# Optimization experiments

Hardware: AMD Instinct MI355X
Metric: run time of the kernel (lower is better)

## Reference

```python
import jax, jax.numpy as jnp
import numpy as np

DIM = 1024
HEADS = 16
HEAD_DIM = DIM // HEADS
EPS = 1e-6


def setup_inputs() -> dict:
    key = jax.random.key(0)
    ks = jax.random.split(key, 4)
    x = jax.random.normal(ks[0], (2, 2048, DIM), dtype=jnp.float32)
    W_qkv = jax.random.normal(ks[1], (3 * DIM, DIM), dtype=jnp.float32) * (DIM ** -0.5)
    q_gamma = jnp.ones((HEAD_DIM,), jnp.float32)
    q_beta = jnp.zeros((HEAD_DIM,), jnp.float32)
    k_gamma = jnp.ones((HEAD_DIM,), jnp.float32)
    k_beta = jnp.zeros((HEAD_DIM,), jnp.float32)
    W_proj = jax.random.normal(ks[2], (DIM, DIM), dtype=jnp.float32) * (DIM ** -0.5)
    b_proj = jnp.zeros((DIM,), jnp.float32)
    return {"x": x, "W_qkv": W_qkv, "q_gamma": q_gamma, "q_beta": q_beta,
            "k_gamma": k_gamma, "k_beta": k_beta, "W_proj": W_proj, "b_proj": b_proj}


def _layernorm(x, gamma, beta):
    mu = jnp.mean(x, axis=-1, keepdims=True)
    var = jnp.mean(jnp.square(x - mu), axis=-1, keepdims=True)
    return (x - mu) * jax.lax.rsqrt(var + EPS) * gamma + beta


def reference(x, W_qkv, q_gamma, q_beta, k_gamma, k_beta, W_proj, b_proj):
    B, N, C = x.shape
    H, D = HEADS, HEAD_DIM
    scale = D ** -0.5
    qkv = jnp.einsum('bnc,oc->bno', x, W_qkv)            # [B,N,3C]
    qkv = qkv.reshape(B, N, 3, H, D).transpose(2, 0, 3, 1, 4)  # [3,B,H,N,D]
    q, k, v = qkv[0], qkv[1], qkv[2]
    q = _layernorm(q, q_gamma, q_beta)
    k = _layernorm(k, k_gamma, k_beta)
    attn = jnp.einsum('bhnd,bhmd->bhnm', q * scale, k)   # [B,H,N,N]
    attn = jax.nn.softmax(attn, axis=-1)
    out = jnp.einsum('bhnm,bhmd->bhnd', attn, v)         # [B,H,N,D]
    out = out.transpose(0, 2, 1, 3).reshape(B, N, C)
    return jnp.einsum('bnc,oc->bno', out, W_proj) + b_proj
```

## Files before the change

### kernel.cpp

```cpp
#include <hip/hip_runtime.h>

#define DIM 1024
#define HEADS 16
#define HD 64
#define BATCH 2
#define SEQ 2048
#define ROWS (BATCH*SEQ)
#define EPS 1e-6f

typedef float f32x4  __attribute__((ext_vector_type(4)));
typedef float f32x16 __attribute__((ext_vector_type(16)));
typedef short s16x4  __attribute__((ext_vector_type(4)));
typedef short s16x8  __attribute__((ext_vector_type(8)));

static __device__ __forceinline__ short f2bf(float f) {
    union { float f; unsigned u; } x; x.f = f;
    unsigned r = x.u + 0x7FFFu + ((x.u >> 16) & 1u);
    return (short)(r >> 16);
}
static __device__ __forceinline__ s16x8 pack8(float4 lo, float4 hi) {
    s16x8 r;
    r[0]=f2bf(lo.x); r[1]=f2bf(lo.y); r[2]=f2bf(lo.z); r[3]=f2bf(lo.w);
    r[4]=f2bf(hi.x); r[5]=f2bf(hi.y); r[6]=f2bf(hi.z); r[7]=f2bf(hi.w);
    return r;
}
static __device__ __forceinline__ unsigned cvtpk(float a, float b) {
    unsigned r;
    asm("v_cvt_pk_bf16_f32 %0, %1, %2" : "=v"(r) : "v"(a), "v"(b));
    return r;
}
static __device__ __forceinline__ void gld16(short* l, const short* g) {
    __builtin_amdgcn_global_load_lds(
        (const __attribute__((address_space(1))) void*)g,
        (__attribute__((address_space(3))) void*)l, 16, 0, 0);
}

#define MFMA32(A,B,C) __builtin_amdgcn_mfma_f32_32x32x16_bf16(A, B, C, 0, 0, 0)
#define MFMA16(A,B,C) __builtin_amdgcn_mfma_f32_16x16x32_bf16(A, B, C, 0, 0, 0)

__global__ __launch_bounds__(256) void convert3(
    const float* __restrict__ x, const float* __restrict__ wq,
    const float* __restrict__ wp,
    short* __restrict__ xb, short* __restrict__ wqb, short* __restrict__ wpb)
{
    const int idx = blockIdx.x * 256 + threadIdx.x;
    const int C1 = 4194304/8, C2 = 3145728/8;
    const float* src; short* dst; int off;
    if (idx < C1)            { src = x;  dst = xb;  off = idx; }
    else if (idx < C1 + C2)  { src = wq; dst = wqb; off = idx - C1; }
    else                     { src = wp; dst = wpb; off = idx - C1 - C2; }
    float4 a = ((const float4*)src)[off*2];
    float4 b = ((const float4*)src)[off*2 + 1];
    ((s16x8*)dst)[off] = pack8(a, b);
}

#define BKG 64

template<int MODE>
__global__ __launch_bounds__(256) void gemm_bf16(
    const short* __restrict__ A, const short* __restrict__ W,
    const float* __restrict__ bias,
    const float* __restrict__ qg, const float* __restrict__ qbeta,
    const float* __restrict__ kg, const float* __restrict__ kbeta,
    short* __restrict__ qb, short* __restrict__ kb, short* __restrict__ vb,
    float* __restrict__ out)
{
    alignas(16) __shared__ short As[128*BKG];
    alignas(16) __shared__ short Bs[128*BKG];
    const int tid  = threadIdx.x;
    const int lane = tid & 63, wave = tid >> 6;
    const int wr = wave >> 1, wc = wave & 1;
    const int c = lane & 15, g = lane >> 4;
    const int brow = blockIdx.y * 128, bcol = blockIdx.x * 128;

    const int srow = lane >> 3;
    const int scol = (lane & 7) * 8;
    const short* ag = A + (size_t)(brow + srow)*DIM + scol;
    const short* wg = W + (size_t)(bcol + srow)*DIM + scol;

    f32x4 acc[4][4] = {};

    for (int k0 = 0; k0 < DIM; k0 += BKG) {
        #pragma unroll
        for (int j = 0; j < 4; j++) {
            const int rg = (wave*4 + j) * 8;
            gld16(&As[rg*BKG], ag + (size_t)rg*DIM + k0);
            gld16(&Bs[rg*BKG], wg + (size_t)rg*DIM + k0);
        }
        __syncthreads();

        #pragma unroll
        for (int ks = 0; ks < 2; ks++) {
            s16x8 af[4], bf[4];
            #pragma unroll
            for (int m = 0; m < 4; m++)
                af[m] = *(const s16x8*)&As[(wr*64 + m*16 + c)*BKG + ks*32 + g*8];
            #pragma unroll
            for (int n = 0; n < 4; n++)
                bf[n] = *(const s16x8*)&Bs[(wc*64 + n*16 + c)*BKG + ks*32 + g*8];
            #pragma unroll
            for (int m = 0; m < 4; m++)
                #pragma unroll
                for (int n = 0; n < 4; n++)
                    acc[m][n] = MFMA16(af[m], bf[n], acc[m][n]);
        }
        __syncthreads();
    }

    if (MODE == 0) {
        const int colbase = bcol + wc*64;
        const int t = colbase >> 10;
        const int h = (colbase >> 6) & 15;
        short* dst = (t == 0) ? qb : (t == 1) ? kb : vb;
        float gam[4], bet[4];
        float scale = 1.0f;
        if (t < 2) {
            const float* G  = (t == 0) ? qg : kg;
            const float* Bt = (t == 0) ? qbeta : kbeta;
            #pragma unroll
            for (int n = 0; n < 4; n++) { gam[n] = G[n*16 + c]; bet[n] = Bt[n*16 + c]; }
            if (t == 0) scale = 0.125f * 1.44269504088896340736f;
        }
        #pragma unroll
        for (int m = 0; m < 4; m++) {
            #pragma unroll
            for (int j = 0; j < 4; j++) {
                const int row = brow + wr*64 + m*16 + g*4 + j;
                const int bi = row >> 11, ni = row & (SEQ-1);
                const size_t rb = ((size_t)(bi*HEADS + h)*SEQ + ni)*HD;
                float v0 = acc[m][0][j], v1 = acc[m][1][j];
                float v2 = acc[m][2][j], v3 = acc[m][3][j];
                if (t < 2) {
                    float s = (v0 + v1) + (v2 + v3);
                    s += __shfl_xor(s, 1); s += __shfl_xor(s, 2);
                    s += __shfl_xor(s, 4); s += __shfl_xor(s, 8);
                    const float mu = s * 0.015625f;
                    v0 -= mu; v1 -= mu; v2 -= mu; v3 -= mu;
                    float vv = (v0*v0 + v1*v1) + (v2*v2 + v3*v3);
                    vv += __shfl_xor(vv, 1); vv += __shfl_xor(vv, 2);
                    vv += __shfl_xor(vv, 4); vv += __shfl_xor(vv, 8);
                    const float rstd = rsqrtf(vv * 0.015625f + EPS);
                    v0 = (v0*rstd*gam[0] + bet[0]) * scale;
                    v1 = (v1*rstd*gam[1] + bet[1]) * scale;
                    v2 = (v2*rstd*gam[2] + bet[2]) * scale;
                    v3 = (v3*rstd*gam[3] + bet[3]) * scale;
                }
                dst[rb + 0*16 + c] = f2bf(v0);
                dst[rb + 1*16 + c] = f2bf(v1);
                dst[rb + 2*16 + c] = f2bf(v2);
                dst[rb + 3*16 + c] = f2bf(v3);
            }
        }
    } else {
        #pragma unroll
        for (int n = 0; n < 4; n++) {
            const int col = bcol + wc*64 + n*16 + c;
            const float bv = bias[col];
            #pragma unroll
            for (int m = 0; m < 4; m++) {
                #pragma unroll
                for (int j = 0; j < 4; j++) {
                    const int row = brow + wr*64 + m*16 + g*4 + j;
                    out[(size_t)row*DIM + col] = acc[m][n][j] + bv;
                }
            }
        }
    }
}

__global__ __launch_bounds__(256) void vtrans(
    const short* __restrict__ vin, short* __restrict__ vt)
{
    constexpr int LT = 72;
    alignas(16) __shared__ short T[64*LT];
    const int bh = blockIdx.x, n0 = blockIdx.y * 64;
    const int t = threadIdx.x;
    const int r = t >> 2, cq = (t & 3) * 16;
    const short* src = vin + ((size_t)bh*SEQ + n0 + r)*HD + cq;
    *(s16x8*)&T[r*LT + cq]     = *(const s16x8*)src;
    *(s16x8*)&T[r*LT + cq + 8] = *(const s16x8*)(src + 8);
    __syncthreads();
    const int d = t >> 2, nq = (t & 3) * 16;
    s16x8 a, b;
    #pragma unroll
    for (int e = 0; e < 8; e++) { a[e] = T[(nq+e)*LT + d]; b[e] = T[(nq+8+e)*LT + d]; }
    short* dst = vt + ((size_t)bh*HD + d)*SEQ + n0 + nq;
    *(s16x8*)dst       = a;
    *(s16x8*)(dst + 8) = b;
}

__global__ __launch_bounds__(512, 4) void attn_kernel(
    const short* __restrict__ qbuf, const short* __restrict__ kbuf,
    const short* __restrict__ vtbuf, short* __restrict__ aout)
{
    alignas(16) __shared__ short Ks[2][2][64*64];
    alignas(16) __shared__ short Vs[2][2][64*64];

    const int bh = blockIdx.x;
    const int tid = threadIdx.x;
    const int wave = tid >> 6, lane = tid & 63;
    const int half = wave >> 2, w4 = wave & 3;
    const int l31 = lane & 31, hi = lane >> 5;
    const int q0 = (blockIdx.y * 4 + w4) * 32;
    const size_t base = (size_t)bh * SEQ * HD;
    const short* Q  = qbuf  + base;
    const short* K  = kbuf  + base;
    const short* VT = vtbuf + base;
    const int kt0 = half * (SEQ/2);

    const int t2 = tid & 255;
    const int srow = t2 >> 2;
    const int scol = (t2 & 3) * 16;
    const int sd0 = (srow*128 + scol*2) ^ ((srow & 7) << 4);
    const int sd1 = sd0 ^ 16;

    s16x8 qf[4];
    const short* qrow = Q + (size_t)(q0 + l31)*HD + 8*hi;
    #pragma unroll
    for (int ks = 0; ks < 4; ks++) qf[ks] = *(const s16x8*)(qrow + 16*ks);

    int roff[8];
    #pragma unroll
    for (int ks = 0; ks < 4; ks++) {
        roff[ks]   = (l31*128      + 32*ks + 16*hi) ^ ((l31 & 7) << 4);
        roff[4+ks] = ((32+l31)*128 + 32*ks + 16*hi) ^ ((l31 & 7) << 4);
    }

    f32x16 o0 = {}, o1 = {};
    float m = -1e30f, l = 0.f;

    {
        const short* kg = K  + (size_t)(kt0 + srow)*HD + scol;
        const short* vg = VT + (size_t)srow*SEQ + kt0 + scol;
        s16x8 ka = *(const s16x8*)kg, kb2 = *(const s16x8*)(kg + 8);
        s16x8 va = *(const s16x8*)vg, vb2 = *(const s16x8*)(vg + 8);
        *(s16x8*)((char*)Ks[half][0] + sd0) = ka;
        *(s16x8*)((char*)Ks[half][0] + sd1) = kb2;
        *(s16x8*)((char*)Vs[half][0] + sd0) = va;
        *(s16x8*)((char*)Vs[half][0] + sd1) = vb2;
    }
    __syncthreads();

    int cur = 0;
    for (int i = 0; i < 16; i++) {
        const int ktn = kt0 + ((i + 1) & 15) * 64;
        const short* kg = K  + (size_t)(ktn + srow)*HD + scol;
        const short* vg = VT + (size_t)srow*SEQ + ktn + scol;
        s16x8 ka = *(const s16x8*)kg, kb2 = *(const s16x8*)(kg + 8);
        s16x8 va = *(const s16x8*)vg, vb2 = *(const s16x8*)(vg + 8);

        const char* kl = (const char*)Ks[half][cur];
        const char* vl = (const char*)Vs[half][cur];

        f32x16 s0 = {}, s1 = {};
        __builtin_amdgcn_s_setprio(1);
        #pragma unroll
        for (int ks = 0; ks < 4; ks++) {
            s16x8 kf0 = *(const s16x8*)(kl + roff[ks]);
            s16x8 kf1 = *(const s16x8*)(kl + roff[4+ks]);
            s0 = MFMA32(kf0, qf[ks], s0);
            s1 = MFMA32(kf1, qf[ks], s1);
        }
        __builtin_amdgcn_s_setprio(0);

        float t8[8];
        #pragma unroll
        for (int i2 = 0; i2 < 8; i2++) t8[i2] = fmaxf(fmaxf(s0[i2], s0[i2+8]), fmaxf(s1[i2], s1[i2+8]));
        #pragma unroll
        for (int i2 = 0; i2 < 4; i2++) t8[i2] = fmaxf(t8[i2], t8[i2+4]);
        float pmax = fmaxf(fmaxf(t8[0], t8[2]), fmaxf(t8[1], t8[3]));
        pmax = fmaxf(pmax, __shfl_xor(pmax, 32));

        if (!__all(pmax - m <= 8.0f)) {
            float mn = fmaxf(m, pmax);
            float corr = exp2f(m - mn);
            #pragma unroll
            for (int i2 = 0; i2 < 16; i2++) { o0[i2] *= corr; o1[i2] *= corr; }
            l *= corr;
            m = mn;
        }
        #pragma unroll
        for (int i2 = 0; i2 < 16; i2++) {
            s0[i2] = exp2f(s0[i2] - m);
            s1[i2] = exp2f(s1[i2] - m);
        }
        float a8[8];
        #pragma unroll
        for (int i2 = 0; i2 < 8; i2++) a8[i2] = (s0[i2] + s0[i2+8]) + (s1[i2] + s1[i2+8]);
        #pragma unroll
        for (int i2 = 0; i2 < 4; i2++) a8[i2] += a8[i2+4];
        float rs = (a8[0] + a8[2]) + (a8[1] + a8[3]);
        rs += __shfl_xor(rs, 32);
        l += rs;

        s16x8 pa[4];
        #pragma unroll
        for (int ks = 0; ks < 4; ks++) {
            const int rb = 8*(ks & 1);
            unsigned A0, A1, B0, B1;
            if (ks < 2) {
                A0 = cvtpk(s0[rb+0], s0[rb+1]); A1 = cvtpk(s0[rb+2], s0[rb+3]);
                B0 = cvtpk(s0[rb+4], s0[rb+5]); B1 = cvtpk(s0[rb+6], s0[rb+7]);
            } else {
                A0 = cvtpk(s1[rb+0], s1[rb+1]); A1 = cvtpk(s1[rb+2], s1[rb+3]);
                B0 = cvtpk(s1[rb+4], s1[rb+5]); B1 = cvtpk(s1[rb+6], s1[rb+7]);
            }
            asm volatile("v_permlane32_swap_b32 %0, %1" : "+v"(A0), "+v"(B0));
            asm volatile("v_permlane32_swap_b32 %0, %1" : "+v"(A1), "+v"(B1));
            union { s16x8 v; unsigned u[4]; } w;
            w.u[0] = A0; w.u[1] = A1; w.u[2] = B0; w.u[3] = B1;
            pa[ks] = w.v;
        }

        __builtin_amdgcn_s_setprio(1);
        #pragma unroll
        for (int ks = 0; ks < 4; ks++) {
            s16x8 vf0 = *(const s16x8*)(vl + roff[ks]);
            s16x8 vf1 = *(const s16x8*)(vl + roff[4+ks]);
            o0 = MFMA32(vf0, pa[ks], o0);
            o1 = MFMA32(vf1, pa[ks], o1);
        }
        __builtin_amdgcn_s_setprio(0);

        const int nxt = cur ^ 1;
        *(s16x8*)((char*)Ks[half][nxt] + sd0) = ka;
        *(s16x8*)((char*)Ks[half][nxt] + sd1) = kb2;
        *(s16x8*)((char*)Vs[half][nxt] + sd0) = va;
        *(s16x8*)((char*)Vs[half][nxt] + sd1) = vb2;
        __syncthreads();
        cur = nxt;
    }

    float* OL = (float*)&Ks[0][0][0];
    float* ML = (float*)&Vs[0][0][0];

    if (half == 1) {
        float* ob = OL + ((size_t)(w4*64 + lane))*32;
        #pragma unroll
        for (int i = 0; i < 8; i++) {
            const int slot = (i + (lane & 7)) & 7;
            f32x4 v;
            if (i < 4) { v[0]=o0[4*i]; v[1]=o0[4*i+1]; v[2]=o0[4*i+2]; v[3]=o0[4*i+3]; }
            else { const int j = i-4; v[0]=o1[4*j]; v[1]=o1[4*j+1]; v[2]=o1[4*j+2]; v[3]=o1[4*j+3]; }
            *(f32x4*)(ob + slot*4) = v;
        }
        ML[w4*64 + lane]       = m;
        ML[256 + w4*64 + lane] = l;
    }
    __syncthreads();
    if (half == 0) {
        const float m1 = ML[w4*64 + lane];
        const float l1 = ML[256 + w4*64 + lane];
        const float ms = fmaxf(m, m1);
        const float c0 = exp2f(m - ms), c1 = exp2f(m1 - ms);
        const float inv = 1.0f / (l*c0 + l1*c1);
        const float* ob = OL + ((size_t)(w4*64 + lane))*32;
        const int b = bh >> 4, h = bh & 15;
        short* dst = aout + ((size_t)(b*SEQ + q0 + l31))*DIM + h*HD;
        #pragma unroll
        for (int i = 0; i < 8; i++) {
            const int slot = (i + (lane & 7)) & 7;
            f32x4 p = *(const f32x4*)(ob + slot*4);
            s16x4 st;
            if (i < 4) {
                #pragma unroll
                for (int j = 0; j < 4; j++) st[j] = f2bf((o0[4*i+j]*c0 + p[j]*c1) * inv);
                *(s16x4*)(dst + 8*i + 4*hi) = st;
            } else {
                const int t3 = i - 4;
                #pragma unroll
                for (int j = 0; j < 4; j++) st[j] = f2bf((o1[4*t3+j]*c0 + p[j]*c1) * inv);
                *(s16x4*)(dst + 32 + 8*t3 + 4*hi) = st;
            }
        }
    }
}

extern "C" void kernel_launch(void* const* d_in, const int* in_sizes, int n_in,
                              void* d_out, int out_size, void* d_ws, size_t ws_size,
                              hipStream_t stream)
{
    const float* x     = (const float*)d_in[0];
    const float* Wqkv  = (const float*)d_in[1];
    const float* qg    = (const float*)d_in[2];
    const float* qbeta = (const float*)d_in[3];
    const float* kg    = (const float*)d_in[4];
    const float* kbeta = (const float*)d_in[5];
    const float* Wproj = (const float*)d_in[6];
    const float* bproj = (const float*)d_in[7];
    float* out = (float*)d_out;

    char* ws = (char*)d_ws;
    const size_t MB = 1024*1024;
    short* xb     = (short*)(ws);
    short* aout   = (short*)(ws);
    short* wqkvb  = (short*)(ws + 8*MB);
    short* wprojb = (short*)(ws + 14*MB);
    short* q      = (short*)(ws + 16*MB);
    short* k      = (short*)(ws + 24*MB);
    short* vrow   = (short*)(ws + 32*MB);
    short* vt     = (short*)(ws + 40*MB);

    convert3<<<dim3(4096), 256, 0, stream>>>(x, Wqkv, Wproj, xb, wqkvb, wprojb);

    gemm_bf16<0><<<dim3(3*DIM/128, ROWS/128), 256, 0, stream>>>(
        xb, wqkvb, nullptr, qg, qbeta, kg, kbeta, q, k, vrow, nullptr);

    vtrans<<<dim3(BATCH*HEADS, SEQ/64), 256, 0, stream>>>(vrow, vt);

    attn_kernel<<<dim3(BATCH*HEADS, SEQ/128), 512, 0, stream>>>(q, k, vt, aout);

    gemm_bf16<1><<<dim3(DIM/128, ROWS/128), 256, 0, stream>>>(
        aout, wprojb, bproj, nullptr, nullptr, nullptr, nullptr,
        nullptr, nullptr, nullptr, out);
}
```

Baseline: 146.3 us.

## Prepack K and V into MFMA fragment order and load directly from global

The V transpose kernel becomes a repack kernel that writes both K and V in per-lane MFMA fragment order, so each lane can fetch its operands with contiguous 16-byte loads. The attention kernel drops its LDS double buffering and per-tile __syncthreads and reads fragments straight from global memory, processing 32-key tiles. Blocks shrink to 256 threads over 64 queries, which doubles the grid. This removes LDS traffic and barriers but gives up cross-wave reuse of K/V through shared memory, relying on L2 and cache hits, and exposes global load latency with no explicit prefetch.

```diff
diff --git a/kernel.cpp b/kernel.cpp
--- a/kernel.cpp
+++ b/kernel.cpp
@@ -168,106 +168,96 @@
     }
 }
 
-__global__ __launch_bounds__(256) void vtrans(
-    const short* __restrict__ vin, short* __restrict__ vt)
+__global__ __launch_bounds__(256) void repack_kv(
+    const short* __restrict__ kin, const short* __restrict__ vin,
+    short* __restrict__ KP, short* __restrict__ VP)
 {
     constexpr int LT = 72;
-    alignas(16) __shared__ short T[64*LT];
+    alignas(16) __shared__ short Kl[64*LT];
+    alignas(16) __shared__ short Vl[64*LT];
     const int bh = blockIdx.x, n0 = blockIdx.y * 64;
-    const int t = threadIdx.x;
-    const int r = t >> 2, cq = (t & 3) * 16;
-    const short* src = vin + ((size_t)bh*SEQ + n0 + r)*HD + cq;
-    *(s16x8*)&T[r*LT + cq]     = *(const s16x8*)src;
-    *(s16x8*)&T[r*LT + cq + 8] = *(const s16x8*)(src + 8);
+    const int tid = threadIdx.x;
+    const int r = tid >> 2, cq = (tid & 3) * 16;
+    {
+        const short* ksrc = kin + ((size_t)bh*SEQ + n0 + r)*HD + cq;
+        const short* vsrc = vin + ((size_t)bh*SEQ + n0 + r)*HD + cq;
+        *(s16x8*)&Kl[r*LT + cq]     = *(const s16x8*)ksrc;
+        *(s16x8*)&Kl[r*LT + cq + 8] = *(const s16x8*)(ksrc + 8);
+        *(s16x8*)&Vl[r*LT + cq]     = *(const s16x8*)vsrc;
+        *(s16x8*)&Vl[r*LT + cq + 8] = *(const s16x8*)(vsrc + 8);
+    }
     __syncthreads();
-    const int d = t >> 2, nq = (t & 3) * 16;
-    s16x8 a, b;
+    const int tt = tid >> 7;
+    const int r2 = tid & 127;
+    const int sub = r2 >> 5, lp = r2 & 31;
+    const size_t tbase = ((size_t)bh*64 + blockIdx.y*2 + tt)*2048 + sub*512;
     #pragma unroll
-    for (int e = 0; e < 8; e++) { a[e] = T[(nq+e)*LT + d]; b[e] = T[(nq+8+e)*LT + d]; }
-    short* dst = vt + ((size_t)bh*HD + d)*SEQ + n0 + nq;
-    *(s16x8*)dst       = a;
-    *(s16x8*)(dst + 8) = b;
-}
-
-__global__ __launch_bounds__(512, 4) void attn_kernel(
-    const short* __restrict__ qbuf, const short* __restrict__ kbuf,
-    const short* __restrict__ vtbuf, short* __restrict__ aout)
-{
-    alignas(16) __shared__ short Ks[2][2][64*64];
-    alignas(16) __shared__ short Vs[2][2][64*64];
-
-    const int bh = blockIdx.x;
-    const int tid = threadIdx.x;
-    const int wave = tid >> 6, lane = tid & 63;
-    const int half = wave >> 2, w4 = wave & 3;
+    for (int g2 = 0; g2 < 2; g2++) {
+        const int lane = 2*lp + g2;
+        s16x8 val = *(const s16x8*)&Kl[(tt*32 + (lane & 31))*LT + sub*16 + 8*(lane >> 5)];
+        *(s16x8*)&KP[tbase + lane*8] = val;
+    }
+    #pragma unroll
+    for (int g2 = 0; g2 < 2; g2++) {
+        const int lane = 2*lp + g2;
+        const int hi = lane >> 5, l31 = lane & 31;
+        s16x8 val;
+        #pragma unroll
+        for (int e = 0; e < 8; e++)
+            val[e] = Vl[(tt*32 + (sub >> 1)*16 + 8*hi + e)*LT + (sub & 1)*32 + l31];
+        *(s16x8*)&VP[tbase + lane*8] = val;
+    }
+}
+
+__global__ __launch_bounds__(256) void attn_kernel(
+    const short* __restrict__ qbuf, const short* __restrict__ KP,
+    const short* __restrict__ VP, short* __restrict__ aout)
+{
+    alignas(16) __shared__ float OL[2][64][32];
+    __shared__ float ML[2][2][64];
+
+    const int bh = blockIdx.x, qt = blockIdx.y;
+    const int tid = threadIdx.x, wave = tid >> 6, lane = tid & 63;
+    const int qsub = wave >> 1, half = wave & 1;
     const int l31 = lane & 31, hi = lane >> 5;
-    const int q0 = (blockIdx.y * 4 + w4) * 32;
-    const size_t base = (size_t)bh * SEQ * HD;
-    const short* Q  = qbuf  + base;
-    const short* K  = kbuf  + base;
-    const short* VT = vtbuf + base;
-    const int kt0 = half * (SEQ/2);
-
-    const int t2 = tid & 255;
-    const int srow = t2 >> 2;
-    const int scol = (t2 & 3) * 16;
-    const int sd0 = (srow*128 + scol*2) ^ ((srow & 7) << 4);
-    const int sd1 = sd0 ^ 16;
+    const int q0 = qt*64 + qsub*32;
 
     s16x8 qf[4];
-    const short* qrow = Q + (size_t)(q0 + l31)*HD + 8*hi;
+    const short* qrow = qbuf + ((size_t)bh*SEQ + q0 + l31)*HD + 8*hi;
     #pragma unroll
     for (int ks = 0; ks < 4; ks++) qf[ks] = *(const s16x8*)(qrow + 16*ks);
 
-    int roff[8];
-    #pragma unroll
-    for (int ks = 0; ks < 4; ks++) {
-        roff[ks]   = (l31*128      + 32*ks + 16*hi) ^ ((l31 & 7) << 4);
-        roff[4+ks] = ((32+l31)*128 + 32*ks + 16*hi) ^ ((l31 & 7) << 4);
-    }
+    const short* kp = KP + ((size_t)bh*64 + half*32)*2048 + lane*8;
+    const short* vp = VP + ((size_t)bh*64 + half*32)*2048 + lane*8;
 
     f32x16 o0 = {}, o1 = {};
     float m = -1e30f, l = 0.f;
 
-    {
-        const short* kg = K  + (size_t)(kt0 + srow)*HD + scol;
-        const short* vg = VT + (size_t)srow*SEQ + kt0 + scol;
-        s16x8 ka = *(const s16x8*)kg, kb2 = *(const s16x8*)(kg + 8);
-        s16x8 va = *(const s16x8*)vg, vb2 = *(const s16x8*)(vg + 8);
-        *(s16x8*)((char*)Ks[half][0] + sd0) = ka;
-        *(s16x8*)((char*)Ks[half][0] + sd1) = kb2;
-        *(s16x8*)((char*)Vs[half][0] + sd0) = va;
-        *(s16x8*)((char*)Vs[half][0] + sd1) = vb2;
-    }
-    __syncthreads();
-
-    int cur = 0;
-    for (int i = 0; i < 16; i++) {
-        const int ktn = kt0 + ((i + 1) & 15) * 64;
-        const short* kg = K  + (size_t)(ktn + srow)*HD + scol;
-        const short* vg = VT + (size_t)srow*SEQ + ktn + scol;
-        s16x8 ka = *(const s16x8*)kg, kb2 = *(const s16x8*)(kg + 8);
-        s16x8 va = *(const s16x8*)vg, vb2 = *(const s16x8*)(vg + 8);
-
-        const char* kl = (const char*)Ks[half][cur];
-        const char* vl = (const char*)Vs[half][cur];
-
-        f32x16 s0 = {}, s1 = {};
+    for (int it = 0; it < 32; it++) {
+        s16x8 kc0 = *(const s16x8*)(kp);
+        s16x8 kc1 = *(const s16x8*)(kp + 512);
+        s16x8 kc2 = *(const s16x8*)(kp + 1024);
+        s16x8 kc3 = *(const s16x8*)(kp + 1536);
+        s16x8 vc0 = *(const s16x8*)(vp);
+        s16x8 vc1 = *(const s16x8*)(vp + 512);
+        s16x8 vc2 = *(const s16x8*)(vp + 1024);
+        s16x8 vc3 = *(const s16x8*)(vp + 1536);
+        kp += 2048; vp += 2048;
+        __builtin_amdgcn_sched_barrier(0);
+
+        f32x16 s = {};
         __builtin_amdgcn_s_setprio(1);
-        #pragma unroll
-        for (int ks = 0; ks < 4; ks++) {
-            s16x8 kf0 = *(const s16x8*)(kl + roff[ks]);
-            s16x8 kf1 = *(const s16x8*)(kl + roff[4+ks]);
-            s0 = MFMA32(kf0, qf[ks], s0);
-            s1 = MFMA32(kf1, qf[ks], s1);
-        }
+        s = MFMA32(kc0, qf[0], s);
+        s = MFMA32(kc1, qf[1], s);
+        s = MFMA32(kc2, qf[2], s);
+        s = MFMA32(kc3, qf[3], s);
         __builtin_amdgcn_s_setprio(0);
 
         float t8[8];
         #pragma unroll
-        for (int i2 = 0; i2 < 8; i2++) t8[i2] = fmaxf(fmaxf(s0[i2], s0[i2+8]), fmaxf(s1[i2], s1[i2+8]));
-        #pragma unroll
-        for (int i2 = 0; i2 < 4; i2++) t8[i2] = fmaxf(t8[i2], t8[i2+4]);
+        for (int i = 0; i < 8; i++) t8[i] = fmaxf(s[i], s[i+8]);
+        #pragma unroll
+        for (int i = 0; i < 4; i++) t8[i] = fmaxf(t8[i], t8[i+4]);
         float pmax = fmaxf(fmaxf(t8[0], t8[2]), fmaxf(t8[1], t8[3]));
         pmax = fmaxf(pmax, __shfl_xor(pmax, 32));
 
@@ -275,67 +265,49 @@
             float mn = fmaxf(m, pmax);
             float corr = exp2f(m - mn);
             #pragma unroll
-            for (int i2 = 0; i2 < 16; i2++) { o0[i2] *= corr; o1[i2] *= corr; }
+            for (int i = 0; i < 16; i++) { o0[i] *= corr; o1[i] *= corr; }
             l *= corr;
             m = mn;
         }
         #pragma unroll
-        for (int i2 = 0; i2 < 16; i2++) {
-            s0[i2] = exp2f(s0[i2] - m);
-            s1[i2] = exp2f(s1[i2] - m);
-        }
+        for (int i = 0; i < 16; i++) s[i] = exp2f(s[i] - m);
         float a8[8];
         #pragma unroll
-        for (int i2 = 0; i2 < 8; i2++) a8[i2] = (s0[i2] + s0[i2+8]) + (s1[i2] + s1[i2+8]);
-        #pragma unroll
-        for (int i2 = 0; i2 < 4; i2++) a8[i2] += a8[i2+4];
+        for (int i = 0; i < 8; i++) a8[i] = s[i] + s[i+8];
+        #pragma unroll
+        for (int i = 0; i < 4; i++) a8[i] += a8[i+4];
         float rs = (a8[0] + a8[2]) + (a8[1] + a8[3]);
         rs += __shfl_xor(rs, 32);
         l += rs;
 
-        s16x8 pa[4];
-        #pragma unroll
-        for (int ks = 0; ks < 4; ks++) {
-            const int rb = 8*(ks & 1);
-            unsigned A0, A1, B0, B1;
-            if (ks < 2) {
-                A0 = cvtpk(s0[rb+0], s0[rb+1]); A1 = cvtpk(s0[rb+2], s0[rb+3]);
-                B0 = cvtpk(s0[rb+4], s0[rb+5]); B1 = cvtpk(s0[rb+6], s0[rb+7]);
-            } else {
-                A0 = cvtpk(s1[rb+0], s1[rb+1]); A1 = cvtpk(s1[rb+2], s1[rb+3]);
-                B0 = cvtpk(s1[rb+4], s1[rb+5]); B1 = cvtpk(s1[rb+6], s1[rb+7]);
-            }
+        s16x8 pa0, pa1;
+        {
+            unsigned A0 = cvtpk(s[0], s[1]),  A1 = cvtpk(s[2], s[3]);
+            unsigned B0 = cvtpk(s[4], s[5]),  B1 = cvtpk(s[6], s[7]);
             asm volatile("v_permlane32_swap_b32 %0, %1" : "+v"(A0), "+v"(B0));
             asm volatile("v_permlane32_swap_b32 %0, %1" : "+v"(A1), "+v"(B1));
             union { s16x8 v; unsigned u[4]; } w;
-            w.u[0] = A0; w.u[1] = A1; w.u[2] = B0; w.u[3] = B1;
-            pa[ks] = w.v;
+            w.u[0]=A0; w.u[1]=A1; w.u[2]=B0; w.u[3]=B1;
+            pa0 = w.v;
+            unsigned C0 = cvtpk(s[8], s[9]),  C1 = cvtpk(s[10], s[11]);
+            unsigned D0 = cvtpk(s[12], s[13]),D1 = cvtpk(s[14], s[15]);
+            asm volatile("v_permlane32_swap_b32 %0, %1" : "+v"(C0), "+v"(D0));
+            asm volatile("v_permlane32_swap_b32 %0, %1" : "+v"(C1), "+v"(D1));
+            union { s16x8 v; unsigned u[4]; } w2;
+            w2.u[0]=C0; w2.u[1]=C1; w2.u[2]=D0; w2.u[3]=D1;
+            pa1 = w2.v;
         }
 
         __builtin_amdgcn_s_setprio(1);
-        #pragma unroll
-        for (int ks = 0; ks < 4; ks++) {
-            s16x8 vf0 = *(const s16x8*)(vl + roff[ks]);
-            s16x8 vf1 = *(const s16x8*)(vl + roff[4+ks]);
-            o0 = MFMA32(vf0, pa[ks], o0);
-            o1 = MFMA32(vf1, pa[ks], o1);
-        }
+        o0 = MFMA32(vc0, pa0, o0);
+        o1 = MFMA32(vc1, pa0, o1);
+        o0 = MFMA32(vc2, pa1, o0);
+        o1 = MFMA32(vc3, pa1, o1);
         __builtin_amdgcn_s_setprio(0);
-
-        const int nxt = cur ^ 1;
-        *(s16x8*)((char*)Ks[half][nxt] + sd0) = ka;
-        *(s16x8*)((char*)Ks[half][nxt] + sd1) = kb2;
-        *(s16x8*)((char*)Vs[half][nxt] + sd0) = va;
-        *(s16x8*)((char*)Vs[half][nxt] + sd1) = vb2;
-        __syncthreads();
-        cur = nxt;
-    }
-
-    float* OL = (float*)&Ks[0][0][0];
-    float* ML = (float*)&Vs[0][0][0];
+    }
 
     if (half == 1) {
-        float* ob = OL + ((size_t)(w4*64 + lane))*32;
+        float* ob = &OL[qsub][lane][0];
         #pragma unroll
         for (int i = 0; i < 8; i++) {
             const int slot = (i + (lane & 7)) & 7;
@@ -344,17 +316,17 @@
             else { const int j = i-4; v[0]=o1[4*j]; v[1]=o1[4*j+1]; v[2]=o1[4*j+2]; v[3]=o1[4*j+3]; }
             *(f32x4*)(ob + slot*4) = v;
         }
-        ML[w4*64 + lane]       = m;
-        ML[256 + w4*64 + lane] = l;
+        ML[qsub][0][lane] = m;
+        ML[qsub][1][lane] = l;
     }
     __syncthreads();
     if (half == 0) {
-        const float m1 = ML[w4*64 + lane];
-        const float l1 = ML[256 + w4*64 + lane];
+        const float m1 = ML[qsub][0][lane];
+        const float l1 = ML[qsub][1][lane];
         const float ms = fmaxf(m, m1);
         const float c0 = exp2f(m - ms), c1 = exp2f(m1 - ms);
         const float inv = 1.0f / (l*c0 + l1*c1);
-        const float* ob = OL + ((size_t)(w4*64 + lane))*32;
+        const float* ob = &OL[qsub][lane][0];
         const int b = bh >> 4, h = bh & 15;
         short* dst = aout + ((size_t)(b*SEQ + q0 + l31))*DIM + h*HD;
         #pragma unroll
@@ -393,22 +365,23 @@
     char* ws = (char*)d_ws;
     const size_t MB = 1024*1024;
     short* xb     = (short*)(ws);
-    short* aout   = (short*)(ws);
+    short* KP     = (short*)(ws);
     short* wqkvb  = (short*)(ws + 8*MB);
     short* wprojb = (short*)(ws + 14*MB);
     short* q      = (short*)(ws + 16*MB);
     short* k      = (short*)(ws + 24*MB);
+    short* aout   = (short*)(ws + 24*MB);
     short* vrow   = (short*)(ws + 32*MB);
-    short* vt     = (short*)(ws + 40*MB);
+    short* VP     = (short*)(ws + 40*MB);
 
     convert3<<<dim3(4096), 256, 0, stream>>>(x, Wqkv, Wproj, xb, wqkvb, wprojb);
 
     gemm_bf16<0><<<dim3(3*DIM/128, ROWS/128), 256, 0, stream>>>(
         xb, wqkvb, nullptr, qg, qbeta, kg, kbeta, q, k, vrow, nullptr);
 
-    vtrans<<<dim3(BATCH*HEADS, SEQ/64), 256, 0, stream>>>(vrow, vt);
-
-    attn_kernel<<<dim3(BATCH*HEADS, SEQ/128), 512, 0, stream>>>(q, k, vt, aout);
+    repack_kv<<<dim3(BATCH*HEADS, SEQ/64), 256, 0, stream>>>(k, vrow, KP, VP);
+
+    attn_kernel<<<dim3(BATCH*HEADS, SEQ/64), 256, 0, stream>>>(q, KP, VP, aout);
 
     gemm_bf16<1><<<dim3(DIM/128, ROWS/128), 256, 0, stream>>>(
         aout, wprojb, bproj, nullptr, nullptr, nullptr, nullptr,
```

New measurement: 150.3 us. 2.7% more time.
